# Optimization experiments

Hardware: AMD Instinct MI355X
Metric: run time of the kernel (lower is better)

The kernel has to match this reference:

```python
import jax, jax.numpy as jnp
import numpy as np

B, T, I, H = 512, 256, 64, 512
HN = 30  # hidden_nodes
EPS = 1e-5


def setup_inputs() -> dict:
    key = jax.random.key(0)
    ks = jax.random.split(key, 14)
    s = 0.05
    return {
        "x": jax.random.normal(ks[0], (B, T, I), jnp.float32),
        "W_ih": jax.random.normal(ks[1], (4 * H, I), jnp.float32) * s,
        "W_hh": jax.random.normal(ks[2], (4 * H, H), jnp.float32) * s,
        "b_ih": jax.random.normal(ks[3], (4 * H,), jnp.float32) * s,
        "b_hh": jax.random.normal(ks[4], (4 * H,), jnp.float32) * s,
        "l1_w": jax.random.normal(ks[5], (HN, H), jnp.float32) * s,
        "l1_b": jax.random.normal(ks[6], (HN,), jnp.float32) * s,
        "l2_w": jax.random.normal(ks[7], (HN, HN), jnp.float32) * s,
        "l3_w": jax.random.normal(ks[8], (HN, HN), jnp.float32) * s,
        "l4_w": jax.random.normal(ks[9], (HN, HN), jnp.float32) * s,
        "l5_w": jax.random.normal(ks[10], (2, HN), jnp.float32) * s,
        "bn_gamma": jnp.ones((HN,), jnp.float32),
        "bn_beta": jnp.zeros((HN,), jnp.float32),
    }


def _bn(a, gamma, beta):
    # training-mode BatchNorm1d: batch statistics over axis 0 (biased var)
    m = jnp.mean(a, axis=0)
    v = jnp.mean((a - m) ** 2, axis=0)
    return gamma * (a - m) * jax.lax.rsqrt(v + EPS) + beta


def reference(x, W_ih, W_hh, b_ih, b_hh, l1_w, l1_b, l2_w, l3_w, l4_w, l5_w,
              bn_gamma, bn_beta):
    def mlp(h):
        a = _bn(h @ l1_w.T + l1_b, bn_gamma, bn_beta)
        a = jax.nn.relu(a)
        a = jax.nn.relu(_bn(a @ l2_w.T, bn_gamma, bn_beta))
        a = jax.nn.relu(_bn(a @ l3_w.T, bn_gamma, bn_beta))
        a = jax.nn.relu(_bn(a @ l4_w.T, bn_gamma, bn_beta))
        return a @ l5_w.T  # [B, 2]

    def step(carry, x_t):
        h, c = carry
        gates = x_t @ W_ih.T + b_ih + h @ W_hh.T + b_hh  # [B, 4H]
        i_g, f_g, g_g, o_g = jnp.split(gates, 4, axis=1)  # torch order: i,f,g,o
        c = jax.nn.sigmoid(f_g) * c + jax.nn.sigmoid(i_g) * jnp.tanh(g_g)
        h = jax.nn.sigmoid(o_g) * jnp.tanh(c)
        return (h, c), mlp(h)

    h0 = jnp.zeros((x.shape[0], H), x.dtype)
    c0 = jnp.zeros((x.shape[0], H), x.dtype)
    xs = jnp.swapaxes(x, 0, 1)  # [T, B, I]
    _, outs = jax.lax.scan(step, (h0, c0), xs)  # [T, B, 2]
    return jnp.transpose(outs, (1, 2, 0))  # [B, 2, T]
```

## Files before the change

### kernel.cpp

```cpp
#include <hip/hip_runtime.h>
#include <math.h>

#define B_  512
#define T_  256
#define I_  64
#define H_  512
#define G4  2048
#define K_  576
#define HN  30
#define EPSf 1e-5f
#define GW  16
#define NG  16
#define BM  32
#define BJ  32
#define KP  584
#define A1P 32
#define HROT 4

typedef __attribute__((ext_vector_type(8))) short short8;
typedef __attribute__((ext_vector_type(4))) float f32x4;

static __device__ __forceinline__ unsigned short f2bf(float f) {
    unsigned int u = __float_as_uint(f);
    u += 0x7fffu + ((u >> 16) & 1u);
    return (unsigned short)(u >> 16);
}
static __device__ __forceinline__ float sigf(float x) {
    return __builtin_amdgcn_rcpf(1.0f + __expf(-x));
}
static __device__ __forceinline__ float tanh_f(float x) {
    float e = __expf(-2.0f * fabsf(x));
    float r = (1.0f - e) * __builtin_amdgcn_rcpf(1.0f + e);
    return copysignf(r, x);
}

__global__ void pack_kernel(const float* __restrict__ x, const float* __restrict__ Wih,
                            const float* __restrict__ Whh, const float* __restrict__ bih,
                            const float* __restrict__ bhh, const float* __restrict__ l1w,
                            unsigned short* __restrict__ Wp, unsigned short* __restrict__ xb,
                            float* __restrict__ bias, unsigned short* __restrict__ hb,
                            float* __restrict__ a1p, unsigned short* __restrict__ wl1b,
                            unsigned int* __restrict__ arr, unsigned int* __restrict__ map) {
    const int stride = gridDim.x * blockDim.x;
    const int g0 = blockIdx.x * blockDim.x + threadIdx.x;
    for (int idx = g0; idx < G4 * K_; idx += stride) {
        int n = idx / K_, k = idx - n * K_;
        float v = (k < H_) ? Whh[n * H_ + k] : Wih[n * I_ + (k - H_)];
        Wp[idx] = f2bf(v);
    }
    for (int idx = g0; idx < T_ * B_ * I_; idx += stride) {
        int t = idx / (B_ * I_);
        int r = idx - t * (B_ * I_);
        int b = r / I_, i = r - b * I_;
        xb[idx] = f2bf(x[((size_t)b * T_ + t) * I_ + i]);
    }
    for (int idx = g0; idx < G4; idx += stride) bias[idx] = bih[idx] + bhh[idx];
    for (int idx = g0; idx < B_ * H_; idx += stride) hb[idx] = 0;
    for (int idx = g0; idx < T_ * B_ * A1P; idx += stride) a1p[idx] = 0.0f;
    for (int idx = g0; idx < 32 * H_; idx += stride) {
        int f = idx >> 9, k = idx & 511;
        wl1b[idx] = (f < HN) ? f2bf(l1w[f * H_ + k]) : 0;
    }
    for (int idx = g0; idx < NG * 64; idx += stride) arr[idx] = 0u;
    for (int idx = g0; idx < 256; idx += stride) map[idx] = 0u;
}

__global__ __launch_bounds__(256, 1) void lstm_kernel(
        const unsigned short* __restrict__ Wp, const unsigned short* __restrict__ xb,
        const float* __restrict__ bias, unsigned short* __restrict__ hb,
        float* __restrict__ a1p, const unsigned short* __restrict__ wl1b,
        unsigned int* __restrict__ arr, unsigned int* __restrict__ map) {
    __shared__ unsigned short As[BM][KP];
    __shared__ unsigned short hsb[BM][40];
    __shared__ int flagLDS;

    const int tid  = threadIdx.x;
    const int w    = tid >> 6;
    const int lane = tid & 63;
    const int r    = lane & 15;
    const int q    = lane >> 4;
    const int mt   = w >> 1;
    const int jt   = w & 1;
    const int mb   = blockIdx.x & 15;
    const int jb   = blockIdx.x >> 4;
    const int m0   = mb * BM;
    const int j0   = jb * BJ;
    const int hrow = tid >> 3, hseg = tid & 7;
    const int mt_l1 = w >> 1, ft_l1 = w & 1;

    if (tid == 0) {
        unsigned xcc;
        asm volatile("s_getreg_b32 %0, hwreg(HW_REG_XCC_ID)" : "=s"(xcc));
        __hip_atomic_store(&map[blockIdx.x], 0x100u | (xcc & 0xffu),
                           __ATOMIC_RELAXED, __HIP_MEMORY_SCOPE_AGENT);
    }

    short8 bfrag[4][18];
#pragma unroll
    for (int g = 0; g < 4; ++g)
#pragma unroll
        for (int kc = 0; kc < 18; ++kc) {
            bfrag[g][kc] = *reinterpret_cast<const short8*>(
                Wp + (size_t)(g * H_ + j0 + jt * 16 + r) * K_ + kc * 32 + q * 8);
            asm volatile("" : "+v"(bfrag[g][kc]));
        }
    short8 bl1 = *reinterpret_cast<const short8*>(
        wl1b + (size_t)(ft_l1 * 16 + r) * H_ + j0 + q * 8);
    asm volatile("" : "+v"(bl1));

    float bias_g[4];
#pragma unroll
    for (int g = 0; g < 4; ++g) bias_g[g] = bias[g * H_ + j0 + jt * 16 + r];

    float c[4] = {0.f, 0.f, 0.f, 0.f};
    unsigned int* ctrA = arr + mb * 64;
    unsigned int* ctrB = arr + mb * 64 + 32;
    int fastf = 0;

#pragma unroll 1
    for (int t = 0; t < T_; ++t) {
        const unsigned short* hin = hb + (size_t)(t % HROT) * B_ * H_;
        unsigned short* hout      = hb + (size_t)((t + 1) % HROT) * B_ * H_;

        const short8 xv = *reinterpret_cast<const short8*>(
            xb + ((size_t)t * B_ + m0 + hrow) * I_ + hseg * 8);

        if (t > 0) {
            if (tid == 0) {
                if (fastf) {
                    const unsigned target = (unsigned)(GW * (t - 1));
                    unsigned tries = 0;
                    for (;;) {
                        unsigned old, zero = 0;
                        asm volatile("global_atomic_add %0, %1, %2, off sc0\n\t"
                                     "s_waitcnt vmcnt(0)"
                                     : "=&v"(old) : "v"(ctrB), "v"(zero) : "memory");
                        if (old >= target) break;
                        if (++tries > 100000u) break;
                        __builtin_amdgcn_s_sleep(1);
                    }
                } else {
                    const unsigned target = (unsigned)(GW * t);
                    unsigned tries = 0;
                    while (__hip_atomic_load(ctrA, __ATOMIC_RELAXED,
                                             __HIP_MEMORY_SCOPE_AGENT) < target) {
                        if (++tries > 100000u) break;
                        __builtin_amdgcn_s_sleep(1);
                    }
                    if (t == 1) {
                        unsigned v0 = __hip_atomic_load(&map[mb], __ATOMIC_RELAXED,
                                                        __HIP_MEMORY_SCOPE_AGENT);
                        int same = (v0 & 0x100u) ? 1 : 0;
                        for (int u = 1; u < GW; ++u) {
                            unsigned vu = __hip_atomic_load(&map[u * 16 + mb],
                                                            __ATOMIC_RELAXED,
                                                            __HIP_MEMORY_SCOPE_AGENT);
                            same &= (vu == v0);
                        }
                        flagLDS = same;
                    }
                }
            }
            __syncthreads();
            if (t == 1) fastf = flagLDS;
            asm volatile("" ::: "memory");
        }

        short8 hv[8];
        const unsigned short* hbase = hin + (size_t)(m0 + hrow) * H_ + hseg * 8;
        if (fastf) {
#pragma unroll
            for (int u = 0; u < 8; ++u)
                asm volatile("global_load_dwordx4 %0, %1, off sc0"
                             : "=&v"(hv[u]) : "v"(hbase + u * 64));
        } else {
#pragma unroll
            for (int u = 0; u < 8; ++u) {
                unsigned long long p2[2];
                p2[0] = __hip_atomic_load((const unsigned long long*)(hbase + u * 64),
                                          __ATOMIC_RELAXED, __HIP_MEMORY_SCOPE_AGENT);
                p2[1] = __hip_atomic_load((const unsigned long long*)(hbase + u * 64 + 4),
                                          __ATOMIC_RELAXED, __HIP_MEMORY_SCOPE_AGENT);
                __builtin_memcpy(&hv[u], p2, 16);
            }
        }
        asm volatile("s_waitcnt vmcnt(0)" ::: "memory");
        __builtin_amdgcn_sched_barrier(0);
        *reinterpret_cast<short8*>(&As[hrow][512 + hseg * 8]) = xv;
#pragma unroll
        for (int u = 0; u < 8; ++u)
            *reinterpret_cast<short8*>(&As[hrow][u * 64 + hseg * 8]) = hv[u];
        __syncthreads();

        f32x4 acc[4];
#pragma unroll
        for (int g = 0; g < 4; ++g)
            acc[g] = (f32x4){bias_g[g], bias_g[g], bias_g[g], bias_g[g]};
#pragma unroll
        for (int kc = 0; kc < 18; ++kc) {
            const short8 afr = *reinterpret_cast<const short8*>(
                &As[mt * 16 + r][kc * 32 + q * 8]);
#pragma unroll
            for (int g = 0; g < 4; ++g)
                acc[g] = __builtin_amdgcn_mfma_f32_16x16x32_bf16(
                    afr, bfrag[g][kc], acc[g], 0, 0, 0);
        }

#pragma unroll
        for (int rr = 0; rr < 4; ++rr) {
            float ig = acc[0][rr], fg = acc[1][rr], gg = acc[2][rr], og = acc[3][rr];
            float cn = sigf(fg) * c[rr] + sigf(ig) * tanh_f(gg);
            c[rr] = cn;
            hsb[mt * 16 + q * 4 + rr][jt * 16 + r] = f2bf(sigf(og) * tanh_f(cn));
        }
        __syncthreads();

        {
            unsigned long long pv;
            __builtin_memcpy(&pv, &hsb[hrow][hseg * 4], 8);
            unsigned long long* hdst = (unsigned long long*)(hout
                + (size_t)(m0 + hrow) * H_ + j0 + hseg * 4);
            if (fastf) *hdst = pv;
            else __hip_atomic_store(hdst, pv, __ATOMIC_RELAXED,
                                    __HIP_MEMORY_SCOPE_AGENT);
        }

        if (t + 1 < T_) {
            asm volatile("s_waitcnt vmcnt(0)" ::: "memory");
            __syncthreads();
            if (tid == 0) {
                if (fastf) {
                    unsigned one = 1;
                    asm volatile("global_atomic_add %0, %1, off"
                                 :: "v"(ctrB), "v"(one) : "memory");
                } else {
                    __hip_atomic_fetch_add(ctrA, 1u, __ATOMIC_RELAXED,
                                           __HIP_MEMORY_SCOPE_AGENT);
                }
            }
        } else {
            __syncthreads();
        }

        const short8 ah = *reinterpret_cast<const short8*>(&hsb[mt_l1 * 16 + r][q * 8]);
        f32x4 d = __builtin_amdgcn_mfma_f32_16x16x32_bf16(
            ah, bl1, (f32x4){0.f, 0.f, 0.f, 0.f}, 0, 0, 0);
        const int f = ft_l1 * 16 + r;
        if (f < HN) {
            float* dst = a1p + ((size_t)t * B_ + m0 + mt_l1 * 16 + q * 4) * A1P + f;
            if (fastf) {
#pragma unroll
                for (int rr = 0; rr < 4; ++rr) {
                    float* p = dst + rr * A1P;
                    asm volatile("global_atomic_add_f32 %0, %1, off"
                                 :: "v"(p), "v"(d[rr]) : "memory");
                }
            } else {
#pragma unroll
                for (int rr = 0; rr < 4; ++rr)
                    __hip_atomic_fetch_add(dst + rr * A1P, d[rr], __ATOMIC_RELAXED,
                                           __HIP_MEMORY_SCOPE_AGENT);
            }
        }
    }
}

static __device__ __forceinline__ void bn_relu30(float v[HN], const float* __restrict__ gamma,
                                                 const float* __restrict__ beta,
                                                 float (*pS)[HN], float (*pQ)[HN]) {
    float s0[HN], s1[HN];
#pragma unroll
    for (int f = 0; f < HN; ++f) { s0[f] = v[f]; s1[f] = v[f] * v[f]; }
#pragma unroll
    for (int off = 32; off >= 1; off >>= 1) {
#pragma unroll
        for (int f = 0; f < HN; ++f) {
            s0[f] += __shfl_xor(s0[f], off);
            s1[f] += __shfl_xor(s1[f], off);
        }
    }
    const int lane = threadIdx.x & 63, w = threadIdx.x >> 6;
    if (lane == 0) {
#pragma unroll
        for (int f = 0; f < HN; ++f) { pS[w][f] = s0[f]; pQ[w][f] = s1[f]; }
    }
    __syncthreads();
#pragma unroll
    for (int f = 0; f < HN; ++f) {
        float S = 0.f, Q = 0.f;
#pragma unroll
        for (int u = 0; u < 8; ++u) { S += pS[u][f]; Q += pQ[u][f]; }
        float m = S * (1.0f / 512.0f);
        float var = Q * (1.0f / 512.0f) - m * m;
        float inv = 1.0f / sqrtf(var + EPSf);
        float tv = gamma[f] * (v[f] - m) * inv + beta[f];
        v[f] = fmaxf(tv, 0.f);
    }
    __syncthreads();
}

static __device__ __forceinline__ void layer30(float v[HN], const float* __restrict__ w) {
    float u[HN];
#pragma unroll
    for (int f = 0; f < HN; ++f) {
        float a = 0.f;
#pragma unroll
        for (int k = 0; k < HN; ++k) a = fmaf(v[k], w[f * HN + k], a);
        u[f] = a;
    }
#pragma unroll
    for (int f = 0; f < HN; ++f) v[f] = u[f];
}

__global__ __launch_bounds__(512) void mlp_kernel(
        const float* __restrict__ a1p, const float* __restrict__ l1b,
        const float* __restrict__ l2w, const float* __restrict__ l3w,
        const float* __restrict__ l4w, const float* __restrict__ l5w,
        const float* __restrict__ gamma, const float* __restrict__ beta,
        float* __restrict__ out) {
    const int t = blockIdx.x;
    const int b = threadIdx.x;
    __shared__ float pS[8][HN], pQ[8][HN];
    float v[HN];
    const float* src = a1p + ((size_t)t * B_ + b) * A1P;
#pragma unroll
    for (int f = 0; f < HN; ++f) v[f] = src[f] + l1b[f];
    bn_relu30(v, gamma, beta, pS, pQ);
    layer30(v, l2w); bn_relu30(v, gamma, beta, pS, pQ);
    layer30(v, l3w); bn_relu30(v, gamma, beta, pS, pQ);
    layer30(v, l4w); bn_relu30(v, gamma, beta, pS, pQ);
    float o0 = 0.f, o1 = 0.f;
#pragma unroll
    for (int k = 0; k < HN; ++k) {
        o0 = fmaf(v[k], l5w[k], o0);
        o1 = fmaf(v[k], l5w[HN + k], o1);
    }
    out[(size_t)b * (2 * T_) + t]      = o0;
    out[(size_t)b * (2 * T_) + T_ + t] = o1;
}

extern "C" void kernel_launch(void* const* d_in, const int* in_sizes, int n_in,
                              void* d_out, int out_size, void* d_ws, size_t ws_size,
                              hipStream_t stream) {
    const float* x    = (const float*)d_in[0];
    const float* Wih  = (const float*)d_in[1];
    const float* Whh  = (const float*)d_in[2];
    const float* bih  = (const float*)d_in[3];
    const float* bhh  = (const float*)d_in[4];
    const float* l1w  = (const float*)d_in[5];
    const float* l1b  = (const float*)d_in[6];
    const float* l2w  = (const float*)d_in[7];
    const float* l3w  = (const float*)d_in[8];
    const float* l4w  = (const float*)d_in[9];
    const float* l5w  = (const float*)d_in[10];
    const float* gam  = (const float*)d_in[11];
    const float* bet  = (const float*)d_in[12];
    float* out = (float*)d_out;

    char* ws = (char*)d_ws;
    unsigned short* Wp   = (unsigned short*)ws;  ws += (size_t)G4 * K_ * 2;
    unsigned short* xb   = (unsigned short*)ws;  ws += (size_t)T_ * B_ * I_ * 2;
    float*          bia  = (float*)ws;           ws += (size_t)G4 * 4;
    unsigned short* hb   = (unsigned short*)ws;  ws += (size_t)HROT * B_ * H_ * 2;
    float*          a1p  = (float*)ws;           ws += (size_t)T_ * B_ * A1P * 4;
    unsigned short* wl1b = (unsigned short*)ws;  ws += (size_t)32 * H_ * 2;
    unsigned int*   arr  = (unsigned int*)ws;    ws += (size_t)NG * 64 * 4;
    unsigned int*   map  = (unsigned int*)ws;    ws += (size_t)256 * 4;

    pack_kernel<<<1024, 256, 0, stream>>>(x, Wih, Whh, bih, bhh, l1w,
                                          Wp, xb, bia, hb, a1p, wl1b, arr, map);
    lstm_kernel<<<NG * GW, 256, 0, stream>>>(Wp, xb, bia, hb, a1p, wl1b, arr, map);
    mlp_kernel<<<T_, 512, 0, stream>>>(a1p, l1b, l2w, l3w, l4w, l5w, gam, bet, out);
}
```

Measured before the change: 952.1 us.

## Retile LSTM blocks to 16 batch rows by 64 hidden units with 8-block sync groups

Each block now covers 16 batch rows and 64 hidden columns instead of 32×32, with one wave per 16-column slice of the gates. The per-timestep barrier group shrinks from 16 to 32 groups of 8 blocks, and each block reads half as much of the previous hidden state. The x-input contribution is now loaded straight into MFMA fragments from global memory rather than staged through LDS. In exchange, the layer-1 projection is split across two K halves, which doubles the atomic adds into a1p.

```diff
diff --git a/kernel.cpp b/kernel.cpp
--- a/kernel.cpp
+++ b/kernel.cpp
@@ -9,11 +9,11 @@
 #define K_  576
 #define HN  30
 #define EPSf 1e-5f
-#define GW  16
-#define NG  16
-#define BM  32
-#define BJ  32
-#define KP  584
+#define GW  8
+#define NG  32
+#define BM  16
+#define BJ  64
+#define KP  520
 #define A1P 32
 #define HROT 4
 
@@ -71,7 +71,7 @@
         float* __restrict__ a1p, const unsigned short* __restrict__ wl1b,
         unsigned int* __restrict__ arr, unsigned int* __restrict__ map) {
     __shared__ unsigned short As[BM][KP];
-    __shared__ unsigned short hsb[BM][40];
+    __shared__ unsigned short hsb[BM][72];
     __shared__ int flagLDS;
 
     const int tid  = threadIdx.x;
@@ -79,14 +79,12 @@
     const int lane = tid & 63;
     const int r    = lane & 15;
     const int q    = lane >> 4;
-    const int mt   = w >> 1;
-    const int jt   = w & 1;
-    const int mb   = blockIdx.x & 15;
-    const int jb   = blockIdx.x >> 4;
+    const int mb   = blockIdx.x & 31;
+    const int jb   = blockIdx.x >> 5;
     const int m0   = mb * BM;
     const int j0   = jb * BJ;
-    const int hrow = tid >> 3, hseg = tid & 7;
-    const int mt_l1 = w >> 1, ft_l1 = w & 1;
+    const int hrow = tid >> 4, hseg = tid & 15;
+    const int ft_l1 = w >> 1, kt_l1 = w & 1;
 
     if (tid == 0) {
         unsigned xcc;
@@ -101,16 +99,16 @@
 #pragma unroll
         for (int kc = 0; kc < 18; ++kc) {
             bfrag[g][kc] = *reinterpret_cast<const short8*>(
-                Wp + (size_t)(g * H_ + j0 + jt * 16 + r) * K_ + kc * 32 + q * 8);
+                Wp + (size_t)(g * H_ + j0 + w * 16 + r) * K_ + kc * 32 + q * 8);
             asm volatile("" : "+v"(bfrag[g][kc]));
         }
     short8 bl1 = *reinterpret_cast<const short8*>(
-        wl1b + (size_t)(ft_l1 * 16 + r) * H_ + j0 + q * 8);
+        wl1b + (size_t)(ft_l1 * 16 + r) * H_ + j0 + kt_l1 * 32 + q * 8);
     asm volatile("" : "+v"(bl1));
 
     float bias_g[4];
 #pragma unroll
-    for (int g = 0; g < 4; ++g) bias_g[g] = bias[g * H_ + j0 + jt * 16 + r];
+    for (int g = 0; g < 4; ++g) bias_g[g] = bias[g * H_ + j0 + w * 16 + r];
 
     float c[4] = {0.f, 0.f, 0.f, 0.f};
     unsigned int* ctrA = arr + mb * 64;
@@ -121,9 +119,6 @@
     for (int t = 0; t < T_; ++t) {
         const unsigned short* hin = hb + (size_t)(t % HROT) * B_ * H_;
         unsigned short* hout      = hb + (size_t)((t + 1) % HROT) * B_ * H_;
-
-        const short8 xv = *reinterpret_cast<const short8*>(
-            xb + ((size_t)t * B_ + m0 + hrow) * I_ + hseg * 8);
 
         if (t > 0) {
             if (tid == 0) {
@@ -152,7 +147,7 @@
                                                         __HIP_MEMORY_SCOPE_AGENT);
                         int same = (v0 & 0x100u) ? 1 : 0;
                         for (int u = 1; u < GW; ++u) {
-                            unsigned vu = __hip_atomic_load(&map[u * 16 + mb],
+                            unsigned vu = __hip_atomic_load(&map[u * 32 + mb],
                                                             __ATOMIC_RELAXED,
                                                             __HIP_MEMORY_SCOPE_AGENT);
                             same &= (vu == v0);
@@ -166,30 +161,33 @@
             asm volatile("" ::: "memory");
         }
 
-        short8 hv[8];
+        const unsigned short* xr = xb + ((size_t)t * B_ + m0 + r) * I_ + q * 8;
+        const short8 xf0 = *reinterpret_cast<const short8*>(xr);
+        const short8 xf1 = *reinterpret_cast<const short8*>(xr + 32);
+
+        short8 hv[4];
         const unsigned short* hbase = hin + (size_t)(m0 + hrow) * H_ + hseg * 8;
         if (fastf) {
 #pragma unroll
-            for (int u = 0; u < 8; ++u)
+            for (int u = 0; u < 4; ++u)
                 asm volatile("global_load_dwordx4 %0, %1, off sc0"
-                             : "=&v"(hv[u]) : "v"(hbase + u * 64));
+                             : "=&v"(hv[u]) : "v"(hbase + u * 128));
         } else {
 #pragma unroll
-            for (int u = 0; u < 8; ++u) {
+            for (int u = 0; u < 4; ++u) {
                 unsigned long long p2[2];
-                p2[0] = __hip_atomic_load((const unsigned long long*)(hbase + u * 64),
+                p2[0] = __hip_atomic_load((const unsigned long long*)(hbase + u * 128),
                                           __ATOMIC_RELAXED, __HIP_MEMORY_SCOPE_AGENT);
-                p2[1] = __hip_atomic_load((const unsigned long long*)(hbase + u * 64 + 4),
+                p2[1] = __hip_atomic_load((const unsigned long long*)(hbase + u * 128 + 4),
                                           __ATOMIC_RELAXED, __HIP_MEMORY_SCOPE_AGENT);
                 __builtin_memcpy(&hv[u], p2, 16);
             }
         }
         asm volatile("s_waitcnt vmcnt(0)" ::: "memory");
         __builtin_amdgcn_sched_barrier(0);
-        *reinterpret_cast<short8*>(&As[hrow][512 + hseg * 8]) = xv;
-#pragma unroll
-        for (int u = 0; u < 8; ++u)
-            *reinterpret_cast<short8*>(&As[hrow][u * 64 + hseg * 8]) = hv[u];
+#pragma unroll
+        for (int u = 0; u < 4; ++u)
+            *reinterpret_cast<short8*>(&As[hrow][u * 128 + hseg * 8]) = hv[u];
         __syncthreads();
 
         f32x4 acc[4];
@@ -197,13 +195,18 @@
         for (int g = 0; g < 4; ++g)
             acc[g] = (f32x4){bias_g[g], bias_g[g], bias_g[g], bias_g[g]};
 #pragma unroll
-        for (int kc = 0; kc < 18; ++kc) {
+        for (int kc = 0; kc < 16; ++kc) {
             const short8 afr = *reinterpret_cast<const short8*>(
-                &As[mt * 16 + r][kc * 32 + q * 8]);
+                &As[r][kc * 32 + q * 8]);
 #pragma unroll
             for (int g = 0; g < 4; ++g)
                 acc[g] = __builtin_amdgcn_mfma_f32_16x16x32_bf16(
                     afr, bfrag[g][kc], acc[g], 0, 0, 0);
+        }
+#pragma unroll
+        for (int g = 0; g < 4; ++g) {
+            acc[g] = __builtin_amdgcn_mfma_f32_16x16x32_bf16(xf0, bfrag[g][16], acc[g], 0, 0, 0);
+            acc[g] = __builtin_amdgcn_mfma_f32_16x16x32_bf16(xf1, bfrag[g][17], acc[g], 0, 0, 0);
         }
 
 #pragma unroll
@@ -211,7 +214,7 @@
             float ig = acc[0][rr], fg = acc[1][rr], gg = acc[2][rr], og = acc[3][rr];
             float cn = sigf(fg) * c[rr] + sigf(ig) * tanh_f(gg);
             c[rr] = cn;
-            hsb[mt * 16 + q * 4 + rr][jt * 16 + r] = f2bf(sigf(og) * tanh_f(cn));
+            hsb[q * 4 + rr][w * 16 + r] = f2bf(sigf(og) * tanh_f(cn));
         }
         __syncthreads();
 
@@ -242,12 +245,13 @@
             __syncthreads();
         }
 
-        const short8 ah = *reinterpret_cast<const short8*>(&hsb[mt_l1 * 16 + r][q * 8]);
+        const short8 ah = *reinterpret_cast<const short8*>(
+            &hsb[r][kt_l1 * 32 + q * 8]);
         f32x4 d = __builtin_amdgcn_mfma_f32_16x16x32_bf16(
             ah, bl1, (f32x4){0.f, 0.f, 0.f, 0.f}, 0, 0, 0);
         const int f = ft_l1 * 16 + r;
         if (f < HN) {
-            float* dst = a1p + ((size_t)t * B_ + m0 + mt_l1 * 16 + q * 4) * A1P + f;
+            float* dst = a1p + ((size_t)t * B_ + m0 + q * 4) * A1P + f;
             if (fastf) {
 #pragma unroll
                 for (int rr = 0; rr < 4; ++rr) {
```

Measured after the change: 907.8 us, median of 2. 4.6% less time.
